# Optimization experiments

Hardware: AMD Instinct MI355X
Metric: run time of the kernel (lower is better)

## Reference

```python
import jax, jax.numpy as jnp
import numpy as np

B, H, C = 131072, 16, 32        # batch, n_holidays, n_changepoints
HID, HP, SKU = 512, 512 // 16, 64  # hidden_dim, hidden per holiday, sku embed dim
TEMP = 0.7
TIME_MAX = 365.0
LN_EPS = 1e-3  # keras LayerNormalization default epsilon


def mish(x):
    return x * jnp.tanh(jax.nn.softplus(x))


def setup_inputs() -> dict:
    key = jax.random.key(0)
    ks = jax.random.split(key, 12)
    inputs = jax.random.uniform(ks[0], (B, H), dtype=jnp.float32) * TIME_MAX
    sku_embedding = jax.random.normal(ks[1], (B, SKU), dtype=jnp.float32)
    # per-holiday params, stacked over holiday axis
    deltas = jnp.full((H, C), TIME_MAX / C, dtype=jnp.float32)  # changepoint_deltas init
    ln_gamma = jnp.ones((H, C), dtype=jnp.float32)
    ln_beta = jnp.zeros((H, C), dtype=jnp.float32)
    attn_w = jax.random.normal(ks[2], (H,), dtype=jnp.float32) * 0.5  # Dense(1) on [...,1]
    Wh = jax.random.normal(ks[3], (H, C, HP), dtype=jnp.float32) * (1.0 / np.sqrt(C))
    Wah = jax.random.normal(ks[4], (HID, HID), dtype=jnp.float32) * (1.0 / np.sqrt(HID))
    Waa = jax.random.normal(ks[5], (HID, HID), dtype=jnp.float32) * (1.0 / np.sqrt(HID))
    Wb = jax.random.normal(ks[6], (SKU, HID), dtype=jnp.float32) * (1.0 / np.sqrt(SKU))
    Wa = jax.random.normal(ks[7], (SKU, HID), dtype=jnp.float32) * (1.0 / np.sqrt(SKU))
    Wo = jax.random.normal(ks[8], (HID, 1), dtype=jnp.float32)
    Wo = Wo / jnp.linalg.norm(Wo, axis=0, keepdims=True)  # UnitNorm(axis=0) constraint
    return {"inputs": inputs, "sku_embedding": sku_embedding, "deltas": deltas,
            "ln_gamma": ln_gamma, "ln_beta": ln_beta, "attn_w": attn_w, "Wh": Wh,
            "Wah": Wah, "Waa": Waa, "Wb": Wb, "Wa": Wa, "Wo": Wo}


def reference(inputs, sku_embedding, deltas, ln_gamma, ln_beta, attn_w, Wh, Wah, Waa, Wb, Wa, Wo):
    # ChangepointReLU (vectorised over holidays): softplus -> cumsum -> rescale to [0, 365]
    pd = jax.nn.softplus(deltas)                     # [H, C]
    cps = jnp.cumsum(pd, axis=-1)
    cps = cps / cps[:, -1:] * TIME_MAX               # time_min = 0
    feats = jax.nn.relu(inputs[:, :, None] - cps[None, :, :])  # [B, H, C]
    # per-holiday LayerNorm over changepoint axis
    mu = jnp.mean(feats, axis=-1, keepdims=True)
    var = jnp.mean((feats - mu) ** 2, axis=-1, keepdims=True)
    normed = (feats - mu) * jax.lax.rsqrt(var + LN_EPS) * ln_gamma[None] + ln_beta[None]
    # per-holiday attention: Dense(1,no bias) on [...,1] == scalar multiply per holiday
    logits = normed * attn_w[None, :, None]
    attn = jax.nn.softmax(logits / TEMP, axis=-1)    # n_changepoints > 1
    attended = normed * attn                          # [B, H, C]
    # per-holiday hidden Dense(HP, mish, no bias), then concat over holidays
    hid = mish(jnp.einsum('bhc,hcd->bhd', attended, Wh))  # [B, H, HP]
    aggregated = hid.reshape(hid.shape[0], H * HP)        # [B, HID]
    agg_hidden = mish(aggregated @ Wah)                   # [B, HID]
    agg_attn = jax.nn.softmax((agg_hidden @ Waa) / TEMP, axis=-1)
    final = agg_hidden * agg_attn                         # dropout inactive (inference)
    beta = jax.nn.sigmoid(sku_embedding @ Wb)
    alpha = sku_embedding @ Wa
    final = final * beta + alpha
    return final @ Wo                                     # [B, 1]
```

## Files before the change

### kernel.cpp

```cpp
#include <hip/hip_runtime.h>
#include <hip/hip_fp16.h>
#include <stdint.h>

#define B_TOT 131072
#define CHUNK 65536
#define NH 16
#define NC 32
#define HIDD 512

typedef unsigned short u16;
typedef __attribute__((ext_vector_type(8))) short short8;
typedef __attribute__((ext_vector_type(4))) float f32x4;
typedef __attribute__((ext_vector_type(4))) int i32x4;

#define GLLDS(g, l) __builtin_amdgcn_global_load_lds((const __attribute__((address_space(1))) unsigned int*)(g), (__attribute__((address_space(3))) unsigned int*)(l), 16, 0, 0)

__device__ __forceinline__ u16 f2bf(float x){
  unsigned u = __float_as_uint(x);
  u += 0x7fffu + ((u >> 16) & 1u);
  return (u16)(u >> 16);
}
__device__ __forceinline__ float bf2f(u16 b){ return __uint_as_float(((unsigned)b) << 16); }
__device__ __forceinline__ u16 f2h(float x){ __half h = __float2half(x); return *(u16*)&h; }
__device__ __forceinline__ float h2f(u16 b){ __half h; *(u16*)&h = b; return __half2float(h); }
__device__ __forceinline__ float mishf(float x){
  float e = __expf(fminf(x, 30.f));
  float u = 1.f + e;
  float u2 = u * u;
  return x * (u2 - 1.f) / (u2 + 1.f);
}

__global__ void prep_small(const float* __restrict__ deltas, const float* __restrict__ Wa,
                           const float* __restrict__ Wo, float* __restrict__ cps, float* __restrict__ wWo)
{
  const int t = threadIdx.x;
  if (t < NH){
    float cum[NC];
    float run = 0.f;
#pragma unroll
    for (int c = 0; c < NC; c++){
      float d = deltas[t*NC + c];
      float sp = (d > 20.f) ? d : log1pf(__expf(d));
      run += sp; cum[c] = run;
    }
    float s = 365.0f / run;
#pragma unroll
    for (int c = 0; c < NC; c++) cps[t*NC + c] = cum[c] * s;
  } else if (t >= 64 && t < 128){
    const int k = t - 64;
    float s = 0.f;
    for (int n = 0; n < HIDD; n++) s += Wa[k*HIDD + n] * Wo[n];
    wWo[k] = s;
  }
}

__global__ void prep_convert(const float* __restrict__ Wah, const float* __restrict__ Waa,
                             const float* __restrict__ Wb, const float* __restrict__ Wh,
                             u16* __restrict__ WahT, u16* __restrict__ WaaT,
                             u16* __restrict__ WbT, u16* __restrict__ WhT)
{
  int i = blockIdx.x * 256 + threadIdx.x;
  if (i < 262144){ int n = i >> 9, k = i & 511; WahT[i] = f2bf(Wah[k*512 + n]); return; }
  i -= 262144;
  if (i < 262144){ int n = i >> 9, k = i & 511; WaaT[i] = f2bf(Waa[k*512 + n]); return; }
  i -= 262144;
  if (i < 32768){ int n = i >> 6, k = i & 63; WbT[i] = f2bf(Wb[k*512 + n]); return; }
  i -= 32768;
  if (i < 16384){ int h = i >> 10, r = i & 1023, d = r >> 5, c = r & 31;
                  WhT[i] = f2bf(Wh[h*1024 + c*32 + d]); return; }
}

__global__ __launch_bounds__(256) void stage1_kernel(
    const float* __restrict__ inputs, const float* __restrict__ sku,
    const float* __restrict__ ln_g, const float* __restrict__ ln_b,
    const float* __restrict__ attnw, const float* __restrict__ cps,
    const float* __restrict__ wWo, const u16* __restrict__ WhT,
    u16* __restrict__ agg, u16* __restrict__ skub, float* __restrict__ skd)
{
  __shared__ __align__(16) float in_l[256];
  __shared__ __align__(16) float cps_l[512];
  __shared__ __align__(16) float gam_l[512];
  __shared__ __align__(16) float bet_l[512];
  __shared__ float aw_l[16];
  __shared__ __align__(16) u16 at_l[16*16*32];
  __shared__ __align__(16) u16 ot_l[16*512];

  const int t = threadIdx.x;
  const int ln = t & 63;
  const long bb = (long)blockIdx.x * 16;

  in_l[t] = inputs[bb*16 + t];
  cps_l[t] = cps[t];       cps_l[t+256] = cps[t+256];
  gam_l[t] = ln_g[t];      gam_l[t+256] = ln_g[t+256];
  bet_l[t] = ln_b[t];      bet_l[t+256] = ln_b[t+256];
  if (t < 16) aw_l[t] = attnw[t];
  {
    const f32x4 sv = *(const f32x4*)&sku[bb*64 + t*4];
    unsigned lo = (unsigned)f2bf(sv.x) | ((unsigned)f2bf(sv.y) << 16);
    unsigned hi = (unsigned)f2bf(sv.z) | ((unsigned)f2bf(sv.w) << 16);
    unsigned long long v = (unsigned long long)lo | ((unsigned long long)hi << 32);
    *(unsigned long long*)&skub[bb*64 + t*4] = v;
    const f32x4 wv4 = *(const f32x4*)&wWo[(ln & 15)*4];
    float pd = sv.x*wv4.x + sv.y*wv4.y + sv.z*wv4.z + sv.w*wv4.w;
#pragma unroll
    for (int s = 1; s < 16; s <<= 1) pd += __shfl_xor(pd, s);
    if ((ln & 15) == 0) skd[bb + (t >> 4)] = pd;
  }
  __syncthreads();

  const int h = t >> 4, bi = t & 15;
  const float x = in_l[bi*16 + h];
  float nrm[NC], pw[NC];
  float s1 = 0.f;
#pragma unroll
  for (int c = 0; c < NC; c++){ float f = fmaxf(x - cps_l[h*NC + c], 0.f); nrm[c] = f; s1 += f; }
  const float mu = s1 * (1.f/NC);
  float s2 = 0.f;
#pragma unroll
  for (int c = 0; c < NC; c++){ float d = nrm[c] - mu; s2 += d*d; }
  const float rs = rsqrtf(s2 * (1.f/NC) + 1e-3f);
  const float aw = aw_l[h] * (1.0f/0.7f);
  float lmax = -1e30f;
#pragma unroll
  for (int c = 0; c < NC; c++){
    float nv = (nrm[c] - mu) * rs * gam_l[h*NC + c] + bet_l[h*NC + c];
    nrm[c] = nv;
    lmax = fmaxf(lmax, nv * aw);
  }
  float ps = 0.f;
#pragma unroll
  for (int c = 0; c < NC; c++){ float p = __expf(nrm[c]*aw - lmax); pw[c] = p; ps += p; }
  const float invs = 1.f / ps;
#pragma unroll
  for (int c = 0; c < NC; c += 2){
    unsigned pk = (unsigned)f2bf(nrm[c]*pw[c]*invs) | ((unsigned)f2bf(nrm[c+1]*pw[c+1]*invs) << 16);
    *(unsigned*)&at_l[h*512 + bi*32 + c] = pk;
  }
  __syncthreads();

  const int wv = t >> 6;
  const int lrow = ln & 15, lq = ln >> 4;
#pragma unroll
  for (int q = 0; q < 4; q++){
    const int hh = wv*4 + q;
    short8 af  = *(const short8*)&at_l[hh*512 + lrow*32 + lq*8];
    short8 bf0 = *(const short8*)&WhT[hh*1024 + lrow*32 + lq*8];
    short8 bf1 = *(const short8*)&WhT[hh*1024 + (16 + lrow)*32 + lq*8];
    f32x4 acc0 = {0.f,0.f,0.f,0.f}, acc1 = {0.f,0.f,0.f,0.f};
    acc0 = __builtin_amdgcn_mfma_f32_16x16x32_bf16(af, bf0, acc0, 0, 0, 0);
    acc1 = __builtin_amdgcn_mfma_f32_16x16x32_bf16(af, bf1, acc1, 0, 0, 0);
#pragma unroll
    for (int r = 0; r < 4; r++){
      const int br = lq*4 + r;
      ot_l[br*512 + hh*32 + lrow]      = f2bf(mishf(acc0[r]));
      ot_l[br*512 + hh*32 + 16 + lrow] = f2bf(mishf(acc1[r]));
    }
  }
  __syncthreads();
  {
    const int row = t >> 4, c16 = t & 15;
    const i32x4* src = (const i32x4*)&ot_l[row*512 + c16*32];
    i32x4* dst = (i32x4*)&agg[(bb + row)*512 + c16*32];
#pragma unroll
    for (int j = 0; j < 4; j++) dst[j] = src[j];
  }
}

__global__ __launch_bounds__(256, 3) void gemm_bw(
    const u16* __restrict__ A, const u16* __restrict__ Bt,
    const float* __restrict__ Wo, u16* __restrict__ bw)
{
  __shared__ __align__(16) u16 As[2][128*32];
  __shared__ __align__(16) u16 Bs[2][128*32];
  const int t = threadIdx.x, wv = t >> 6, ln = t & 63;
  const int g = blockIdx.x;
  const int m_idx = (g & 7) + ((g >> 5) << 3);
  const int n_idx = (g >> 3) & 3;
  const long m0 = (long)m_idx * 128;
  const int n0 = n_idx * 128;
  const int lrow = ln & 15, lq = ln >> 4;
  const int wm = wv >> 1, wn = wv & 1;

  auto stage = [&](int buf, int kt){
#pragma unroll
    for (int p = 0; p < 2; p++){
      const int chunk = p*256 + wv*64 + ln;
      const int mm = chunk >> 2, kc = chunk & 3;
      const int kcl = kc ^ ((mm >> 1) & 3);
      GLLDS(&A[(m0 + mm)*64 + kt + kcl*8],  &As[buf][(p*256 + wv*64)*8]);
      GLLDS(&Bt[(n0 + mm)*64 + kt + kcl*8], &Bs[buf][(p*256 + wv*64)*8]);
    }
  };

  f32x4 acc[4][4] = {};
  stage(0, 0);
  for (int ks = 0; ks < 2; ks++){
    const int cur = ks & 1;
    __syncthreads();
    if (ks + 1 < 2) stage(cur ^ 1, (ks + 1)*32);
    short8 a[4], b[4];
#pragma unroll
    for (int i = 0; i < 4; i++){
      const int ra = wm*64 + i*16 + lrow;
      const int rb = wn*64 + i*16 + lrow;
      const int lqa = lq ^ ((ra >> 1) & 3);
      const int lqb = lq ^ ((rb >> 1) & 3);
      a[i] = *(const short8*)&As[cur][ra*32 + lqa*8];
      b[i] = *(const short8*)&Bs[cur][rb*32 + lqb*8];
    }
#pragma unroll
    for (int i = 0; i < 4; i++)
#pragma unroll
      for (int j = 0; j < 4; j++)
        acc[i][j] = __builtin_amdgcn_mfma_f32_16x16x32_bf16(a[i], b[j], acc[i][j], 0, 0, 0);
  }
#pragma unroll
  for (int j = 0; j < 4; j++){
    const int n = n0 + wn*64 + j*16 + lrow;
    const float wo = Wo[n];
#pragma unroll
    for (int i = 0; i < 4; i++){
#pragma unroll
      for (int r = 0; r < 4; r++){
        const long m = m0 + wm*64 + i*16 + lq*4 + r;
        const float sig = 1.f / (1.f + __expf(-acc[i][j][r]));
        bw[m*512 + n] = f2h(sig * wo);
      }
    }
  }
}

__global__ __launch_bounds__(512, 2) void gemm_mish(
    const u16* __restrict__ A, const u16* __restrict__ Bt, u16* __restrict__ aggh)
{
  __shared__ __align__(16) u16 lds[2*128*32 + 2*512*32];
  u16* As0 = lds;
  u16* Bs0 = lds + 2*128*32;
  const int t = threadIdx.x, wv = t >> 6, ln = t & 63;
  const int lrow = ln & 15, lq = ln >> 4;
  const int rh = wv >> 2, cq = wv & 3;
  const long m0 = (long)blockIdx.x * 128;

  auto stageA = [&](int buf, int kt){
    const int mm = t >> 2, kc = t & 3;
    const int kcl = kc ^ ((mm >> 1) & 3);
    GLLDS(&A[(m0 + mm)*512 + kt + kcl*8], &As0[buf*4096 + t*8]);
  };
  auto stageB = [&](int buf, int kt){
#pragma unroll
    for (int p = 0; p < 4; p++){
      const int idx = p*512 + t;
      const int mm = idx >> 2, kc = idx & 3;
      const int kcl = kc ^ ((mm >> 1) & 3);
      GLLDS(&Bt[(long)mm*512 + kt + kcl*8], &Bs0[buf*16384 + idx*8]);
    }
  };

  f32x4 acc[4][8] = {};
  stageA(0, 0); stageB(0, 0);
  for (int ks = 0; ks < 16; ks++){
    const int cur = ks & 1;
    __syncthreads();
    if (ks + 1 < 16){ stageA(cur ^ 1, (ks + 1)*32); stageB(cur ^ 1, (ks + 1)*32); }
    short8 a[4], b[8];
#pragma unroll
    for (int i = 0; i < 4; i++){
      const int ra = rh*64 + i*16 + lrow;
      const int lqa = lq ^ ((ra >> 1) & 3);
      a[i] = *(const short8*)&As0[cur*4096 + ra*32 + lqa*8];
    }
#pragma unroll
    for (int j = 0; j < 8; j++){
      const int rb = cq*128 + j*16 + lrow;
      const int lqb = lq ^ ((rb >> 1) & 3);
      b[j] = *(const short8*)&Bs0[cur*16384 + rb*32 + lqb*8];
    }
#pragma unroll
    for (int i = 0; i < 4; i++)
#pragma unroll
      for (int j = 0; j < 8; j++)
        acc[i][j] = __builtin_amdgcn_mfma_f32_16x16x32_bf16(a[i], b[j], acc[i][j], 0, 0, 0);
  }

  const int TP = 528;
  __syncthreads();
#pragma unroll 1
  for (int h = 0; h < 2; h++){
    if (rh == h){
#pragma unroll
      for (int i = 0; i < 4; i++)
#pragma unroll
        for (int j = 0; j < 8; j++)
#pragma unroll
          for (int r = 0; r < 4; r++)
            lds[(i*16 + lq*4 + r)*TP + cq*128 + j*16 + lrow] = f2bf(mishf(acc[i][j][r]));
    }
    __syncthreads();
#pragma unroll
    for (int it = 0; it < 8; it++){
      const int idx = it*512 + t;
      const int row = idx >> 6, off = idx & 63;
      const i32x4 v = *(const i32x4*)&lds[row*TP + off*8];
      *(i32x4*)&aggh[(m0 + h*64 + row)*512 + off*8] = v;
    }
    __syncthreads();
  }
}

__global__ __launch_bounds__(512, 2) void mega2(
    const u16* __restrict__ A, const u16* __restrict__ Bt,
    const u16* __restrict__ bw, const float* __restrict__ skd,
    float* __restrict__ outp)
{
  __shared__ __align__(16) u16 As[2][128*32];
  __shared__ __align__(16) u16 Bs[2][512*32];
  const int t = threadIdx.x, wv = t >> 6, ln = t & 63;
  const int lrow = ln & 15, lq = ln >> 4;
  const int rh = wv >> 2, cq = wv & 3;
  const long m0 = (long)blockIdx.x * 128;

  auto stageA = [&](int buf, int kt){
    const int mm = t >> 2, kc = t & 3;
    const int kcl = kc ^ ((mm >> 1) & 3);
    GLLDS(&A[(m0 + mm)*512 + kt + kcl*8], &As[buf][t*8]);
  };
  auto stageB = [&](int buf, int kt){
#pragma unroll
    for (int p = 0; p < 4; p++){
      const int idx = p*512 + t;
      const int mm = idx >> 2, kc = idx & 3;
      const int kcl = kc ^ ((mm >> 1) & 3);
      GLLDS(&Bt[(long)mm*512 + kt + kcl*8], &Bs[buf][idx*8]);
    }
  };

  f32x4 acc[4][8] = {};
  stageA(0, 0); stageB(0, 0);
  for (int ks = 0; ks < 16; ks++){
    const int cur = ks & 1;
    __syncthreads();
    if (ks + 1 < 16){ stageA(cur ^ 1, (ks + 1)*32); stageB(cur ^ 1, (ks + 1)*32); }
    short8 a[4], b[8];
#pragma unroll
    for (int i = 0; i < 4; i++){
      const int ra = rh*64 + i*16 + lrow;
      const int lqa = lq ^ ((ra >> 1) & 3);
      a[i] = *(const short8*)&As[cur][ra*32 + lqa*8];
    }
#pragma unroll
    for (int j = 0; j < 8; j++){
      const int rb = cq*128 + j*16 + lrow;
      const int lqb = lq ^ ((rb >> 1) & 3);
      b[j] = *(const short8*)&Bs[cur][rb*32 + lqb*8];
    }
#pragma unroll
    for (int i = 0; i < 4; i++)
#pragma unroll
      for (int j = 0; j < 8; j++)
        acc[i][j] = __builtin_amdgcn_mfma_f32_16x16x32_bf16(a[i], b[j], acc[i][j], 0, 0, 0);
  }

  __syncthreads();
  float* mxs = (float*)&Bs[0][0];
  float* sss = mxs + 512;
  float* tts = sss + 512;
  const float inv_t = 1.0f / 0.7f;

#pragma unroll
  for (int i = 0; i < 4; i++){
#pragma unroll
    for (int r = 0; r < 4; r++){
      float tm = acc[i][0][r];
#pragma unroll
      for (int j = 1; j < 8; j++) tm = fmaxf(tm, acc[i][j][r]);
#pragma unroll
      for (int s = 1; s < 16; s <<= 1) tm = fmaxf(tm, __shfl_xor(tm, s));
      if (lrow == 0) mxs[(rh*64 + i*16 + lq*4 + r)*4 + cq] = tm;
    }
  }
  __syncthreads();
#pragma unroll
  for (int i = 0; i < 4; i++){
#pragma unroll
    for (int r = 0; r < 4; r++){
      const int row = rh*64 + i*16 + lq*4 + r;
      const float gm = fmaxf(fmaxf(mxs[row*4+0], mxs[row*4+1]),
                             fmaxf(mxs[row*4+2], mxs[row*4+3]));
      float sp = 0.f, tp = 0.f;
#pragma unroll
      for (int j = 0; j < 8; j++){
        const long gi = (m0 + row)*512 + cq*128 + j*16 + lrow;
        const float e = __expf((acc[i][j][r] - gm) * inv_t);
        sp += e;
        tp += e * bf2f(A[gi]) * h2f(bw[gi]);
      }
#pragma unroll
      for (int s = 1; s < 16; s <<= 1){ sp += __shfl_xor(sp, s); tp += __shfl_xor(tp, s); }
      if (lrow == 0){ sss[row*4 + cq] = sp; tts[row*4 + cq] = tp; }
    }
  }
  __syncthreads();
  if (t < 128){
    const float S = sss[t*4] + sss[t*4+1] + sss[t*4+2] + sss[t*4+3];
    const float T = tts[t*4] + tts[t*4+1] + tts[t*4+2] + tts[t*4+3];
    outp[m0 + t] = T / S + skd[m0 + t];
  }
}

__global__ void ws_too_small(float* o, float v){ o[(long)blockIdx.x*256 + threadIdx.x] = v; }

extern "C" void kernel_launch(void* const* d_in, const int* in_sizes, int n_in,
                              void* d_out, int out_size, void* d_ws, size_t ws_size,
                              hipStream_t stream)
{
  const float* inputs = (const float*)d_in[0];
  const float* sku    = (const float*)d_in[1];
  const float* deltas = (const float*)d_in[2];
  const float* ln_g   = (const float*)d_in[3];
  const float* ln_b   = (const float*)d_in[4];
  const float* attnw  = (const float*)d_in[5];
  const float* Wh     = (const float*)d_in[6];
  const float* Wah    = (const float*)d_in[7];
  const float* Waa    = (const float*)d_in[8];
  const float* Wb     = (const float*)d_in[9];
  const float* Wa     = (const float*)d_in[10];
  const float* Wo     = (const float*)d_in[11];
  float* outp = (float*)d_out;

  const size_t OFF_CPS  = 0;
  const size_t OFF_WWO  = 2048;
  const size_t OFF_WAHT = 4096;
  const size_t OFF_WAAT = OFF_WAHT + 524288;
  const size_t OFF_WBT  = OFF_WAAT + 524288;
  const size_t OFF_WHT  = OFF_WBT  + 65536;
  const size_t OFF_SKUB = OFF_WHT  + 32768;
  const size_t OFF_SKD  = OFF_SKUB + (size_t)CHUNK*64*2;
  const size_t OFF_AGG  = OFF_SKD  + (size_t)CHUNK*4;
  const size_t OFF_BW   = OFF_AGG  + (size_t)CHUNK*512*2;
  const size_t OFF_AGH  = OFF_BW   + (size_t)CHUNK*512*2;
  const size_t NEED     = OFF_AGH  + (size_t)CHUNK*512*2;

  if (ws_size < NEED){
    hipLaunchKernelGGL(ws_too_small, dim3(B_TOT/256), dim3(256), 0, stream,
                       outp, -(float)(ws_size >> 20));
    return;
  }

  char* ws = (char*)d_ws;
  float* cps  = (float*)(ws + OFF_CPS);
  float* wWo  = (float*)(ws + OFF_WWO);
  u16* WahT   = (u16*)(ws + OFF_WAHT);
  u16* WaaT   = (u16*)(ws + OFF_WAAT);
  u16* WbT    = (u16*)(ws + OFF_WBT);
  u16* WhT    = (u16*)(ws + OFF_WHT);
  u16* skub   = (u16*)(ws + OFF_SKUB);
  float* skd  = (float*)(ws + OFF_SKD);
  u16* agg    = (u16*)(ws + OFF_AGG);
  u16* bw     = (u16*)(ws + OFF_BW);
  u16* aggh   = (u16*)(ws + OFF_AGH);

  hipLaunchKernelGGL(prep_small, dim3(1), dim3(128), 0, stream, deltas, Wa, Wo, cps, wWo);
  hipLaunchKernelGGL(prep_convert, dim3(2240), dim3(256), 0, stream,
                     Wah, Waa, Wb, Wh, WahT, WaaT, WbT, WhT);

  for (int ch = 0; ch < B_TOT / CHUNK; ch++){
    const float* in_c  = inputs + (size_t)ch * CHUNK * 16;
    const float* sku_c = sku    + (size_t)ch * CHUNK * 64;
    float* out_c       = outp   + (size_t)ch * CHUNK;

    hipLaunchKernelGGL(stage1_kernel, dim3(CHUNK/16), dim3(256), 0, stream,
                       in_c, sku_c, ln_g, ln_b, attnw, cps, wWo, WhT, agg, skub, skd);
    hipLaunchKernelGGL(gemm_bw, dim3(CHUNK/128*4), dim3(256), 0, stream,
                       skub, WbT, Wo, bw);
    hipLaunchKernelGGL(gemm_mish, dim3(CHUNK/128), dim3(512), 0, stream,
                       agg, WahT, aggh);
    hipLaunchKernelGGL(mega2, dim3(CHUNK/128), dim3(512), 0, stream,
                       aggh, WaaT, bw, skd, out_c);
  }
}
```

Measured before the change: 520.5 us.

## Fuse sku beta GEMM into softmax epilogue of mega2, drop bw buffer

Removes the separate gemm_bw kernel and computes sigmoid(sku@Wb) inside mega2's epilogue with MFMA, staging the sku rows in LDS and reading WbT straight from global. Wo is applied per column in the reduction. This avoids writing and re-reading a 64K×512 fp16 intermediate per chunk and saves one launch per chunk. In exchange, mega2 does extra MFMA and sigmoid work and uncached global loads of WbT, and the loop over i is no longer unrolled, which raises its register pressure and latency.

```diff
diff --git a/kernel.cpp b/kernel.cpp
--- a/kernel.cpp
+++ b/kernel.cpp
@@ -166,70 +166,6 @@
   }
 }
 
-__global__ __launch_bounds__(256, 3) void gemm_bw(
-    const u16* __restrict__ A, const u16* __restrict__ Bt,
-    const float* __restrict__ Wo, u16* __restrict__ bw)
-{
-  __shared__ __align__(16) u16 As[2][128*32];
-  __shared__ __align__(16) u16 Bs[2][128*32];
-  const int t = threadIdx.x, wv = t >> 6, ln = t & 63;
-  const int g = blockIdx.x;
-  const int m_idx = (g & 7) + ((g >> 5) << 3);
-  const int n_idx = (g >> 3) & 3;
-  const long m0 = (long)m_idx * 128;
-  const int n0 = n_idx * 128;
-  const int lrow = ln & 15, lq = ln >> 4;
-  const int wm = wv >> 1, wn = wv & 1;
-
-  auto stage = [&](int buf, int kt){
-#pragma unroll
-    for (int p = 0; p < 2; p++){
-      const int chunk = p*256 + wv*64 + ln;
-      const int mm = chunk >> 2, kc = chunk & 3;
-      const int kcl = kc ^ ((mm >> 1) & 3);
-      GLLDS(&A[(m0 + mm)*64 + kt + kcl*8],  &As[buf][(p*256 + wv*64)*8]);
-      GLLDS(&Bt[(n0 + mm)*64 + kt + kcl*8], &Bs[buf][(p*256 + wv*64)*8]);
-    }
-  };
-
-  f32x4 acc[4][4] = {};
-  stage(0, 0);
-  for (int ks = 0; ks < 2; ks++){
-    const int cur = ks & 1;
-    __syncthreads();
-    if (ks + 1 < 2) stage(cur ^ 1, (ks + 1)*32);
-    short8 a[4], b[4];
-#pragma unroll
-    for (int i = 0; i < 4; i++){
-      const int ra = wm*64 + i*16 + lrow;
-      const int rb = wn*64 + i*16 + lrow;
-      const int lqa = lq ^ ((ra >> 1) & 3);
-      const int lqb = lq ^ ((rb >> 1) & 3);
-      a[i] = *(const short8*)&As[cur][ra*32 + lqa*8];
-      b[i] = *(const short8*)&Bs[cur][rb*32 + lqb*8];
-    }
-#pragma unroll
-    for (int i = 0; i < 4; i++)
-#pragma unroll
-      for (int j = 0; j < 4; j++)
-        acc[i][j] = __builtin_amdgcn_mfma_f32_16x16x32_bf16(a[i], b[j], acc[i][j], 0, 0, 0);
-  }
-#pragma unroll
-  for (int j = 0; j < 4; j++){
-    const int n = n0 + wn*64 + j*16 + lrow;
-    const float wo = Wo[n];
-#pragma unroll
-    for (int i = 0; i < 4; i++){
-#pragma unroll
-      for (int r = 0; r < 4; r++){
-        const long m = m0 + wm*64 + i*16 + lq*4 + r;
-        const float sig = 1.f / (1.f + __expf(-acc[i][j][r]));
-        bw[m*512 + n] = f2h(sig * wo);
-      }
-    }
-  }
-}
-
 __global__ __launch_bounds__(512, 2) void gemm_mish(
     const u16* __restrict__ A, const u16* __restrict__ Bt, u16* __restrict__ aggh)
 {
@@ -309,7 +245,8 @@
 
 __global__ __launch_bounds__(512, 2) void mega2(
     const u16* __restrict__ A, const u16* __restrict__ Bt,
-    const u16* __restrict__ bw, const float* __restrict__ skd,
+    const u16* __restrict__ skub, const u16* __restrict__ WbT,
+    const float* __restrict__ Wo, const float* __restrict__ skd,
     float* __restrict__ outp)
 {
   __shared__ __align__(16) u16 As[2][128*32];
@@ -364,8 +301,19 @@
   float* mxs = (float*)&Bs[0][0];
   float* sss = mxs + 512;
   float* tts = sss + 512;
+  u16* skl   = (u16*)&Bs[0][0] + 4096;
+  const int SP = 72;
   const float inv_t = 1.0f / 0.7f;
 
+  {
+#pragma unroll
+    for (int it = 0; it < 2; it++){
+      const int idx = it*512 + t;
+      const int row = idx >> 3, kc = idx & 7;
+      const short8 v = *(const short8*)&skub[(m0 + row)*64 + kc*8];
+      *(short8*)&skl[row*SP + kc*8] = v;
+    }
+  }
 #pragma unroll
   for (int i = 0; i < 4; i++){
 #pragma unroll
@@ -379,8 +327,19 @@
     }
   }
   __syncthreads();
-#pragma unroll
+
+#pragma unroll 1
   for (int i = 0; i < 4; i++){
+    f32x4 accb[8] = {};
+#pragma unroll
+    for (int ks2 = 0; ks2 < 2; ks2++){
+      const short8 a2 = *(const short8*)&skl[(rh*64 + i*16 + lrow)*SP + ks2*32 + lq*8];
+#pragma unroll
+      for (int j = 0; j < 8; j++){
+        const short8 b2 = *(const short8*)&WbT[(cq*128 + j*16 + lrow)*64 + ks2*32 + lq*8];
+        accb[j] = __builtin_amdgcn_mfma_f32_16x16x32_bf16(a2, b2, accb[j], 0, 0, 0);
+      }
+    }
 #pragma unroll
     for (int r = 0; r < 4; r++){
       const int row = rh*64 + i*16 + lq*4 + r;
@@ -389,10 +348,12 @@
       float sp = 0.f, tp = 0.f;
 #pragma unroll
       for (int j = 0; j < 8; j++){
-        const long gi = (m0 + row)*512 + cq*128 + j*16 + lrow;
+        const int col = cq*128 + j*16 + lrow;
+        const long gi = (m0 + row)*512 + col;
         const float e = __expf((acc[i][j][r] - gm) * inv_t);
+        const float beta = 1.f / (1.f + __expf(-accb[j][r]));
         sp += e;
-        tp += e * bf2f(A[gi]) * h2f(bw[gi]);
+        tp += e * bf2f(A[gi]) * beta * Wo[col];
       }
 #pragma unroll
       for (int s = 1; s < 16; s <<= 1){ sp += __shfl_xor(sp, s); tp += __shfl_xor(tp, s); }
@@ -436,8 +397,7 @@
   const size_t OFF_SKUB = OFF_WHT  + 32768;
   const size_t OFF_SKD  = OFF_SKUB + (size_t)CHUNK*64*2;
   const size_t OFF_AGG  = OFF_SKD  + (size_t)CHUNK*4;
-  const size_t OFF_BW   = OFF_AGG  + (size_t)CHUNK*512*2;
-  const size_t OFF_AGH  = OFF_BW   + (size_t)CHUNK*512*2;
+  const size_t OFF_AGH  = OFF_AGG  + (size_t)CHUNK*512*2;
   const size_t NEED     = OFF_AGH  + (size_t)CHUNK*512*2;
 
   if (ws_size < NEED){
@@ -456,7 +416,6 @@
   u16* skub   = (u16*)(ws + OFF_SKUB);
   float* skd  = (float*)(ws + OFF_SKD);
   u16* agg    = (u16*)(ws + OFF_AGG);
-  u16* bw     = (u16*)(ws + OFF_BW);
   u16* aggh   = (u16*)(ws + OFF_AGH);
 
   hipLaunchKernelGGL(prep_small, dim3(1), dim3(128), 0, stream, deltas, Wa, Wo, cps, wWo);
@@ -470,11 +429,9 @@
 
     hipLaunchKernelGGL(stage1_kernel, dim3(CHUNK/16), dim3(256), 0, stream,
                        in_c, sku_c, ln_g, ln_b, attnw, cps, wWo, WhT, agg, skub, skd);
-    hipLaunchKernelGGL(gemm_bw, dim3(CHUNK/128*4), dim3(256), 0, stream,
-                       skub, WbT, Wo, bw);
     hipLaunchKernelGGL(gemm_mish, dim3(CHUNK/128), dim3(512), 0, stream,
                        agg, WahT, aggh);
     hipLaunchKernelGGL(mega2, dim3(CHUNK/128), dim3(512), 0, stream,
-                       aggh, WaaT, bw, skd, out_c);
-  }
-}
+                       aggh, WaaT, skub, WbT, Wo, skd, out_c);
+  }
+}
```

Result: slower. 1.930 ms (+270.8%).
